# Optimization experiments

Hardware: AMD Instinct MI355X
Metric: run time of the kernel (lower is better)

The kernel has to match this reference:

```python
import jax, jax.numpy as jnp
import numpy as np

N_SESS = 4096
N_TRIALS = 2048


def setup_inputs() -> dict:
    key = jax.random.key(0)
    k1, k2 = jax.random.split(key)
    # chose_left is a one-hot choice; chose_right = 1 - chose_left; outcome in {0,1}
    chose_left = jax.random.bernoulli(k1, 0.5, (N_SESS, N_TRIALS)).astype(jnp.float32)
    chose_right = 1.0 - chose_left
    outcome = jax.random.bernoulli(k2, 0.5, (N_SESS, N_TRIALS)).astype(jnp.float32)
    inp = jnp.stack([chose_left, chose_right, outcome], axis=-1)  # (n_sess, n_trials, 3)
    # raw logits; AlphaParam applies sigmoid. logit(0.8), logit(0.6)
    p_stay_raw = jnp.array([np.log(0.8 / 0.2)], dtype=jnp.float32)
    c_raw = jnp.array([np.log(0.6 / 0.4)], dtype=jnp.float32)
    return {"input": inp, "p_stay_raw": p_stay_raw, "c_raw": c_raw}


def _forward(inp, p_stay_raw, c_raw):
    p = jax.nn.sigmoid(p_stay_raw)[0]
    c = jax.nn.sigmoid(c_raw)[0]
    # With complement_c_rew=complement_c_diff=True, all four c params equal c.
    # ev_mat (4,2): rows = [left&rew, left&unrew, right&rew, right&unrew]
    col0 = 0.5 * jnp.stack([1 + c, 1 - c, 1 - c, 1 + c])
    col1 = 0.5 * jnp.stack([1 - c, 1 + c, 1 + c, 1 - c])
    ev_mat = jnp.stack([col0, col1], axis=1)  # (4, 2)
    trans_mat = 0.5 * jnp.stack([jnp.stack([1 + p, 1 - p]),
                                 jnp.stack([1 - p, 1 + p])])  # (2, 2)

    n_sess = inp.shape[0]
    init_state = jnp.full((n_sess, 2), 0.5, dtype=inp.dtype)

    def step(state, x):  # state: (n_sess, 2), x: (n_sess, 3)
        cl, cr, o = x[:, 0], x[:, 1], x[:, 2]
        sel = jnp.stack([cl * o, cl * (1 - o), cr * o, cr * (1 - o)], axis=1)  # (n_sess, 4)
        evidence = sel @ ev_mat            # (n_sess, 2)
        like = evidence * state            # (n_sess, 2)
        like_sum = like.sum(axis=1)        # (n_sess,)
        zero = like_sum == 0
        like = jnp.where(zero[:, None], state, like)
        like_sum = jnp.where(zero, 1.0, like_sum)
        norm_like = like / like_sum[:, None]
        new_state = norm_like @ trans_mat  # (n_sess, 2)
        return new_state, new_state

    # scan over trials (time axis); output stacked as (n_trials, n_sess, 2)
    _, out = jax.lax.scan(step, init_state, jnp.swapaxes(inp, 0, 1))
    return jnp.swapaxes(out, 0, 1)  # (n_sess, n_trials, 2)


def reference(input, p_stay_raw, c_raw):
    return _forward(input, p_stay_raw, c_raw)
```

## Files before the change

### kernel.cpp

```cpp
#include <hip/hip_runtime.h>
#include <cmath>


constexpr int NSESS   = 4096;
constexpr int NTRIALS = 2048;
constexpr int WAVES   = 4;
constexpr int THREADS = WAVES * 64;
constexpr int TPW     = NTRIALS / WAVES;
constexpr int LCH     = TPW / 64;
constexpr int IN_F4   = NTRIALS * 3 / 4;
constexpr int OUT_F4  = NTRIALS * 2 / 4;

__global__ __launch_bounds__(THREADS) void hmm_kernel(
    const float* __restrict__ inp,
    const float* __restrict__ p_raw,
    const float* __restrict__ c_raw,
    float* __restrict__ out)
{
    __shared__ float4 lds[IN_F4];
    __shared__ float  lds_tot[WAVES][4];

    const int t    = threadIdx.x;
    const int lane = t & 63;
    const int w    = t >> 6;
    const int sess = blockIdx.x;

    const float p = 1.0f / (1.0f + __expf(-p_raw[0]));
    const float c = 1.0f / (1.0f + __expf(-c_raw[0]));
    const float A = 0.5f * (1.0f + c), B = 0.5f * (1.0f - c);
    const float q = 0.5f * (1.0f + p), r = 0.5f * (1.0f - p);

    const float4* g_in = reinterpret_cast<const float4*>(inp) + (size_t)sess * IN_F4;
    #pragma unroll
    for (int k = 0; k < IN_F4 / THREADS; ++k)
        lds[k * THREADS + t] = g_in[k * THREADS + t];
    __syncthreads();

    float e0c[LCH], e1c[LCH];
    float p00 = 1.f, p01 = 0.f, p10 = 0.f, p11 = 1.f;
    {
        float4 v[LCH * 3 / 4];
        const int base = w * (TPW * 3 / 4) + lane * (LCH * 3 / 4);
        #pragma unroll
        for (int k = 0; k < LCH * 3 / 4; ++k) v[k] = lds[base + k];
        const float* f = reinterpret_cast<const float*>(v);
        #pragma unroll
        for (int i = 0; i < LCH; ++i) {
            float cl = f[3 * i], cr = f[3 * i + 1], o = f[3 * i + 2];
            float d0 = cl * o + cr * (1.f - o);
            float d1 = cl * (1.f - o) + cr * o;
            float e0 = d0 * A + d1 * B;
            float e1 = d0 * B + d1 * A;
            e0c[i] = e0; e1c[i] = e1;
            float m00, m01, m10, m11;
            if (e0 == 0.f && e1 == 0.f) { m00 = q; m01 = r; m10 = r; m11 = q; }
            else { m00 = e0 * q; m01 = e0 * r; m10 = e1 * r; m11 = e1 * q; }
            float n00 = p00 * m00 + p01 * m10;
            float n01 = p00 * m01 + p01 * m11;
            float n10 = p10 * m00 + p11 * m10;
            float n11 = p10 * m01 + p11 * m11;
            p00 = n00; p01 = n01; p10 = n10; p11 = n11;
        }
    }

    #pragma unroll
    for (int d = 1; d < 64; d <<= 1) {
        float a00 = __shfl_up(p00, d);
        float a01 = __shfl_up(p01, d);
        float a10 = __shfl_up(p10, d);
        float a11 = __shfl_up(p11, d);
        if (lane >= d) {
            float n00 = a00 * p00 + a01 * p10;
            float n01 = a00 * p01 + a01 * p11;
            float n10 = a10 * p00 + a11 * p10;
            float n11 = a10 * p01 + a11 * p11;
            float inv = 1.f / (n00 + n01 + n10 + n11);
            p00 = n00 * inv; p01 = n01 * inv; p10 = n10 * inv; p11 = n11 * inv;
        }
    }

    if (lane == 63) {
        lds_tot[w][0] = p00; lds_tot[w][1] = p01;
        lds_tot[w][2] = p10; lds_tot[w][3] = p11;
    }
    __syncthreads();

    float v0 = 0.5f, v1 = 0.5f;
    for (int ww = 0; ww < w; ++ww) {
        float t00 = lds_tot[ww][0], t01 = lds_tot[ww][1];
        float t10 = lds_tot[ww][2], t11 = lds_tot[ww][3];
        float n0 = v0 * t00 + v1 * t10;
        float n1 = v0 * t01 + v1 * t11;
        float inv = 1.f / (n0 + n1);
        v0 = n0 * inv; v1 = n1 * inv;
    }
    float c00 = __shfl_up(p00, 1);
    float c01 = __shfl_up(p01, 1);
    float c10 = __shfl_up(p10, 1);
    float c11 = __shfl_up(p11, 1);
    float u0 = v0, u1 = v1;
    if (lane > 0) {
        float n0 = v0 * c00 + v1 * c10;
        float n1 = v0 * c01 + v1 * c11;
        float inv = 1.f / (n0 + n1);
        u0 = n0 * inv; u1 = n1 * inv;
    }

    float4* lds_out = lds;
    #pragma unroll
    for (int i = 0; i < LCH; i += 2) {
        float a0, a1, b0, b1;
        {
            float w0 = u0 * e0c[i], w1 = u1 * e1c[i];
            if (w0 + w1 == 0.f) { w0 = u0; w1 = u1; }
            float n0 = w0 * q + w1 * r;
            float n1 = w0 * r + w1 * q;
            float inv = 1.f / (n0 + n1);
            a0 = n0 * inv; a1 = n1 * inv;
            u0 = n0; u1 = n1;
        }
        {
            float w0 = u0 * e0c[i + 1], w1 = u1 * e1c[i + 1];
            if (w0 + w1 == 0.f) { w0 = u0; w1 = u1; }
            float n0 = w0 * q + w1 * r;
            float n1 = w0 * r + w1 * q;
            float inv = 1.f / (n0 + n1);
            b0 = n0 * inv; b1 = n1 * inv;
            u0 = n0; u1 = n1;
        }
        lds_out[w * 256 + (i >> 1) * 64 + lane] = make_float4(a0, a1, b0, b1);
    }
    __syncthreads();

    float4* g_out = reinterpret_cast<float4*>(out) + (size_t)sess * OUT_F4;
    #pragma unroll
    for (int k = 0; k < OUT_F4 / THREADS; ++k) {
        g_out[k * 256 + t] = lds_out[k * 256 + (t & 3) * 64 + (t >> 2)];
    }
}

extern "C" void kernel_launch(void* const* d_in, const int* in_sizes, int n_in,
                              void* d_out, int out_size, void* d_ws, size_t ws_size,
                              hipStream_t stream) {
    const float* inp   = (const float*)d_in[0];
    const float* p_raw = (const float*)d_in[1];
    const float* c_raw = (const float*)d_in[2];
    float* out = (float*)d_out;

    hmm_kernel<<<dim3(NSESS), dim3(THREADS), 0, stream>>>(inp, p_raw, c_raw, out);
}
```

Measured before the change: 166.9 us.

## Load inputs and store outputs directly from registers, dropping LDS staging

Each thread now reads its six float4 input chunks straight from global memory and writes its four float4 outputs directly, removing the LDS staging buffer and two block barriers. Exact divisions are replaced by the hardware reciprocal intrinsic, and launch bounds now request higher occupancy. The cost is uncoalesced per-thread strided global accesses (96-byte input and 64-byte output spans per lane) and slightly lower reciprocal precision.

```diff
diff --git a/kernel.cpp b/kernel.cpp
--- a/kernel.cpp
+++ b/kernel.cpp
@@ -8,17 +8,18 @@
 constexpr int THREADS = WAVES * 64;
 constexpr int TPW     = NTRIALS / WAVES;
 constexpr int LCH     = TPW / 64;
-constexpr int IN_F4   = NTRIALS * 3 / 4;
-constexpr int OUT_F4  = NTRIALS * 2 / 4;
 
-__global__ __launch_bounds__(THREADS) void hmm_kernel(
+__device__ __forceinline__ float frcp(float x) {
+    return __builtin_amdgcn_rcpf(x);
+}
+
+__global__ __launch_bounds__(THREADS, 8) void hmm_kernel(
     const float* __restrict__ inp,
     const float* __restrict__ p_raw,
     const float* __restrict__ c_raw,
     float* __restrict__ out)
 {
-    __shared__ float4 lds[IN_F4];
-    __shared__ float  lds_tot[WAVES][4];
+    __shared__ float lds_tot[WAVES][4];
 
     const int t    = threadIdx.x;
     const int lane = t & 63;
@@ -30,20 +31,18 @@
     const float A = 0.5f * (1.0f + c), B = 0.5f * (1.0f - c);
     const float q = 0.5f * (1.0f + p), r = 0.5f * (1.0f - p);
 
-    const float4* g_in = reinterpret_cast<const float4*>(inp) + (size_t)sess * IN_F4;
-    #pragma unroll
-    for (int k = 0; k < IN_F4 / THREADS; ++k)
-        lds[k * THREADS + t] = g_in[k * THREADS + t];
-    __syncthreads();
+    const float4* xv = reinterpret_cast<const float4*>(inp)
+                     + (size_t)sess * (NTRIALS * 3 / 4)
+                     + w * (TPW * 3 / 4) + lane * (LCH * 3 / 4);
+    float4 v0 = xv[0], v1 = xv[1], v2 = xv[2];
+    float4 v3 = xv[3], v4 = xv[4], v5 = xv[5];
 
     float e0c[LCH], e1c[LCH];
     float p00 = 1.f, p01 = 0.f, p10 = 0.f, p11 = 1.f;
     {
-        float4 v[LCH * 3 / 4];
-        const int base = w * (TPW * 3 / 4) + lane * (LCH * 3 / 4);
-        #pragma unroll
-        for (int k = 0; k < LCH * 3 / 4; ++k) v[k] = lds[base + k];
-        const float* f = reinterpret_cast<const float*>(v);
+        float f[LCH * 3] = {v0.x, v0.y, v0.z, v0.w, v1.x, v1.y, v1.z, v1.w,
+                            v2.x, v2.y, v2.z, v2.w, v3.x, v3.y, v3.z, v3.w,
+                            v4.x, v4.y, v4.z, v4.w, v5.x, v5.y, v5.z, v5.w};
         #pragma unroll
         for (int i = 0; i < LCH; ++i) {
             float cl = f[3 * i], cr = f[3 * i + 1], o = f[3 * i + 2];
@@ -74,7 +73,7 @@
             float n01 = a00 * p01 + a01 * p11;
             float n10 = a10 * p00 + a11 * p10;
             float n11 = a10 * p01 + a11 * p11;
-            float inv = 1.f / (n00 + n01 + n10 + n11);
+            float inv = frcp(n00 + n01 + n10 + n11);
             p00 = n00 * inv; p01 = n01 * inv; p10 = n10 * inv; p11 = n11 * inv;
         }
     }
@@ -85,28 +84,30 @@
     }
     __syncthreads();
 
-    float v0 = 0.5f, v1 = 0.5f;
+    float s0 = 0.5f, s1 = 0.5f;
     for (int ww = 0; ww < w; ++ww) {
         float t00 = lds_tot[ww][0], t01 = lds_tot[ww][1];
         float t10 = lds_tot[ww][2], t11 = lds_tot[ww][3];
-        float n0 = v0 * t00 + v1 * t10;
-        float n1 = v0 * t01 + v1 * t11;
-        float inv = 1.f / (n0 + n1);
-        v0 = n0 * inv; v1 = n1 * inv;
+        float n0 = s0 * t00 + s1 * t10;
+        float n1 = s0 * t01 + s1 * t11;
+        float inv = frcp(n0 + n1);
+        s0 = n0 * inv; s1 = n1 * inv;
     }
     float c00 = __shfl_up(p00, 1);
     float c01 = __shfl_up(p01, 1);
     float c10 = __shfl_up(p10, 1);
     float c11 = __shfl_up(p11, 1);
-    float u0 = v0, u1 = v1;
+    float u0 = s0, u1 = s1;
     if (lane > 0) {
-        float n0 = v0 * c00 + v1 * c10;
-        float n1 = v0 * c01 + v1 * c11;
-        float inv = 1.f / (n0 + n1);
+        float n0 = s0 * c00 + s1 * c10;
+        float n1 = s0 * c01 + s1 * c11;
+        float inv = frcp(n0 + n1);
         u0 = n0 * inv; u1 = n1 * inv;
     }
 
-    float4* lds_out = lds;
+    float4* yv = reinterpret_cast<float4*>(out)
+               + (size_t)sess * (NTRIALS * 2 / 4) + w * (TPW * 2 / 4) + lane * 4;
+
     #pragma unroll
     for (int i = 0; i < LCH; i += 2) {
         float a0, a1, b0, b1;
@@ -115,7 +116,7 @@
             if (w0 + w1 == 0.f) { w0 = u0; w1 = u1; }
             float n0 = w0 * q + w1 * r;
             float n1 = w0 * r + w1 * q;
-            float inv = 1.f / (n0 + n1);
+            float inv = frcp(n0 + n1);
             a0 = n0 * inv; a1 = n1 * inv;
             u0 = n0; u1 = n1;
         }
@@ -124,18 +125,11 @@
             if (w0 + w1 == 0.f) { w0 = u0; w1 = u1; }
             float n0 = w0 * q + w1 * r;
             float n1 = w0 * r + w1 * q;
-            float inv = 1.f / (n0 + n1);
+            float inv = frcp(n0 + n1);
             b0 = n0 * inv; b1 = n1 * inv;
             u0 = n0; u1 = n1;
         }
-        lds_out[w * 256 + (i >> 1) * 64 + lane] = make_float4(a0, a1, b0, b1);
-    }
-    __syncthreads();
-
-    float4* g_out = reinterpret_cast<float4*>(out) + (size_t)sess * OUT_F4;
-    #pragma unroll
-    for (int k = 0; k < OUT_F4 / THREADS; ++k) {
-        g_out[k * 256 + t] = lds_out[k * 256 + (t & 3) * 64 + (t >> 2)];
+        yv[i >> 1] = make_float4(a0, a1, b0, b1);
     }
 }
 
```

Result: slower. 172.0 us (+3.1%).
